# Kernel tuning notes

Measured on AMD Instinct MI355X. Metric: run time of the kernel, lower is better.

The kernel has to match this reference:

```python
import jax, jax.numpy as jnp
import numpy as np

NEIGH = 0.4  # neighborhood_size from the module


def setup_inputs() -> dict:
    key = jax.random.key(0)
    ks = jax.random.split(key, 14)
    N, E, H, G, M = 1024, 64, 128, 8, 20
    OUT = 6 * M
    f32 = jnp.float32
    inp = {
        "xabs": jax.random.uniform(ks[0], (N, 2), f32),
        "i_h0": jax.random.normal(ks[1], (1, N, H), f32) * 0.1,
        "i_c0": jax.random.normal(ks[2], (1, N, H), f32) * 0.1,
        # I_Embedding: Linear(2, E)
        "W_emb": jax.random.normal(ks[3], (E, 2), f32) * 0.5,
        "b_emb": jax.random.normal(ks[4], (E,), f32) * 0.1,
        # embedding_social: Linear(G*G*H, E)
        "W_soc": jax.random.normal(ks[5], (E, G * G * H), f32) * (1.0 / np.sqrt(G * G * H)),
        "b_soc": jax.random.normal(ks[6], (E,), f32) * 0.1,
        # LSTM(2E -> H), torch gate order [i, f, g, o]
        "W_ih": jax.random.normal(ks[7], (4 * H, 2 * E), f32) * (1.0 / np.sqrt(2 * E)),
        "W_hh": jax.random.normal(ks[8], (4 * H, H), f32) * (1.0 / np.sqrt(H)),
        "b_ih": jax.random.normal(ks[9], (4 * H,), f32) * 0.05,
        "b_hh": jax.random.normal(ks[10], (4 * H,), f32) * 0.05,
        # I_Output: Linear(H, 6*M)
        "W_out": jax.random.normal(ks[11], (OUT, H), f32) * (1.0 / np.sqrt(H)),
        "b_out": jax.random.normal(ks[12], (OUT,), f32) * 0.05,
    }
    return inp


def _grid_mask(xabs, G):
    # Vectorized getGridMask: [N, N, G*G] one-hot bin membership.
    N = xabs.shape[0]
    # dx[n, m] = other_x - width_low(n); in-range iff 0 <= dx < NEIGH
    dx = xabs[None, :, 0] - (xabs[:, None, 0] - NEIGH / 2)
    dy = xabs[None, :, 1] - (xabs[:, None, 1] - NEIGH / 2)
    cell_x = jnp.floor(dx / NEIGH * G).astype(jnp.int32)
    cell_y = jnp.floor(dy / NEIGH * G).astype(jnp.int32)
    valid = (dx >= 0) & (dx < NEIGH) & (dy >= 0) & (dy < NEIGH)
    valid &= (cell_x >= 0) & (cell_x < G) & (cell_y >= 0) & (cell_y < G)
    valid &= ~jnp.eye(N, dtype=bool)  # skip self
    cell = jnp.where(valid, cell_x + cell_y * G, 0)
    mask = jax.nn.one_hot(cell, G * G, dtype=xabs.dtype)
    return mask * valid[:, :, None].astype(xabs.dtype)


def reference(xabs, i_h0, i_c0, W_emb, b_emb, W_soc, b_soc,
              W_ih, W_hh, b_ih, b_hh, W_out, b_out):
    N = xabs.shape[0]
    H = i_h0.shape[-1]
    G = int(np.sqrt(W_soc.shape[1] // H))
    M = W_out.shape[0] // 6

    # Input embedding
    emb_x = jax.nn.relu(xabs @ W_emb.T + b_emb)  # [N, E]

    # Social pooling: grid mask + scatter-reduce of hidden states
    h0 = i_h0[0]  # [N, H]
    mask = _grid_mask(xabs, G)  # [N, N, G*G]
    social = jnp.einsum('nmg,md->ngd', mask, h0)  # [N, G*G, H]
    social = social.reshape(N, G * G * H)
    pooling = jax.nn.relu(social @ W_soc.T + b_soc)  # [N, E]

    # Single LSTM step (seq len 1, 1 layer), torch gate order i,f,g,o
    lstm_in = jnp.concatenate([emb_x, pooling], axis=-1)  # [N, 2E]
    gates = lstm_in @ W_ih.T + b_ih + h0 @ W_hh.T + b_hh  # [N, 4H]
    i_g, f_g, g_g, o_g = jnp.split(gates, 4, axis=-1)
    c = jax.nn.sigmoid(f_g) * i_c0[0] + jax.nn.sigmoid(i_g) * jnp.tanh(g_g)
    h = jax.nn.sigmoid(o_g) * jnp.tanh(c)  # [N, H]

    final = h @ W_out.T + b_out  # [N, 6M]
    mu1, mu2, log_sigma1, log_sigma2, rho, pi_logits = jnp.split(final, 6, axis=1)
    return (mu1, mu2, log_sigma1, log_sigma2, rho, pi_logits)
```

## Files before the change

### kernel.cpp

```cpp
#include <hip/hip_runtime.h>
#include <hip/hip_bf16.h>
#include <math.h>

typedef __hip_bfloat16 bf16;
typedef short s8v __attribute__((ext_vector_type(8)));
typedef float f4v __attribute__((ext_vector_type(4)));

__device__ __forceinline__ float b2f(bf16 v) { return __bfloat162float(v); }

template <bool F32>
__device__ __forceinline__ float ld(const void* p, int i) {
  if (F32) return ((const float*)p)[i];
  return b2f(((const bf16*)p)[i]);
}

template <bool F32>
__device__ __forceinline__ s8v ldfrag(const void* p, size_t i) {
  if (F32) {
    const float* f = (const float*)p + i;
    float4 u = *reinterpret_cast<const float4*>(f);
    float4 v = *reinterpret_cast<const float4*>(f + 4);
    s8v r;
    bf16 t;
    t = __float2bfloat16(u.x); r[0] = *(short*)&t;
    t = __float2bfloat16(u.y); r[1] = *(short*)&t;
    t = __float2bfloat16(u.z); r[2] = *(short*)&t;
    t = __float2bfloat16(u.w); r[3] = *(short*)&t;
    t = __float2bfloat16(v.x); r[4] = *(short*)&t;
    t = __float2bfloat16(v.y); r[5] = *(short*)&t;
    t = __float2bfloat16(v.z); r[6] = *(short*)&t;
    t = __float2bfloat16(v.w); r[7] = *(short*)&t;
    return r;
  }
  return *reinterpret_cast<const s8v*>((const bf16*)p + i);
}

__device__ __forceinline__ float sigm(float x) {
  return 0.5f * (1.0f + tanhf(0.5f * x));
}

__device__ __forceinline__ bool detect_f32(const void* xabs) {
  unsigned short v = ((const unsigned short*)xabs)[threadIdx.x & 63];
  int ex = (v >> 7) & 0xFF;
  return __ballot(ex >= 0x93) != 0ull;
}

template <bool F32>
__device__ __forceinline__ void cvt_f4(const void* src, bf16* __restrict__ dst,
                                       int i4) {
  if (F32) {
    float4 v = reinterpret_cast<const float4*>(src)[i4];
    bf16 t[4] = {__float2bfloat16(v.x), __float2bfloat16(v.y),
                 __float2bfloat16(v.z), __float2bfloat16(v.w)};
    reinterpret_cast<uint2*>(dst)[i4] = *reinterpret_cast<uint2*>(t);
  } else {
    reinterpret_cast<uint2*>(dst)[i4] = reinterpret_cast<const uint2*>(src)[i4];
  }
}

template <bool F32>
__device__ __forceinline__ void zgemm_body(const void* h0, const void* Wsoc,
                                           const void* Wih, const void* Whh,
                                           const void* Wout,
                                           bf16* __restrict__ Z, bf16* Wih_b,
                                           bf16* Whh_b, bf16* Wout_b) {
  const int t4 = blockIdx.x * 256 + threadIdx.x;
  if (t4 < 16384)
    cvt_f4<F32>(Wih, Wih_b, t4);
  else if (t4 < 32768)
    cvt_f4<F32>(Whh, Whh_b, t4 - 16384);
  else if (t4 < 36608)
    cvt_f4<F32>(Wout, Wout_b, t4 - 32768);

  const int wave = threadIdx.x >> 6, lane = threadIdx.x & 63;
  const int mt = blockIdx.x & 15;
  const int g  = (blockIdx.x >> 4) * 4 + wave;
  const int r16 = lane & 15, quad = lane >> 4;

  s8v afr[4][4];
#pragma unroll
  for (int ms = 0; ms < 4; ++ms)
#pragma unroll
    for (int kq = 0; kq < 4; ++kq)
      afr[ms][kq] = ldfrag<F32>(
          h0, (size_t)(mt * 64 + ms * 16 + r16) * 128 + kq * 32 + quad * 8);

  f4v acc[4][4];
#pragma unroll
  for (int ms = 0; ms < 4; ++ms)
#pragma unroll
    for (int t = 0; t < 4; ++t) acc[ms][t] = (f4v){0.f, 0.f, 0.f, 0.f};

#pragma unroll
  for (int t = 0; t < 4; ++t) {
#pragma unroll
    for (int kq = 0; kq < 4; ++kq) {
      s8v bfr = ldfrag<F32>(
          Wsoc, (size_t)(t * 16 + r16) * 8192 + g * 128 + kq * 32 + quad * 8);
#pragma unroll
      for (int ms = 0; ms < 4; ++ms)
        acc[ms][t] = __builtin_amdgcn_mfma_f32_16x16x32_bf16(afr[ms][kq], bfr,
                                                             acc[ms][t], 0, 0, 0);
    }
  }
#pragma unroll
  for (int ms = 0; ms < 4; ++ms)
#pragma unroll
    for (int t = 0; t < 4; ++t)
#pragma unroll
      for (int reg = 0; reg < 4; ++reg)
        Z[(size_t)(mt * 64 + ms * 16 + quad * 4 + reg) * 4096 + g * 64 +
          t * 16 + r16] = __float2bfloat16(acc[ms][t][reg]);
}

__global__ __launch_bounds__(256, 1) void k_zgemm(
    const void* h0, const void* Wsoc, const void* Wih, const void* Whh,
    const void* Wout, bf16* __restrict__ Z, bf16* Wih_b, bf16* Whh_b,
    bf16* Wout_b, const void* xabs) {
  if (detect_f32(xabs))
    zgemm_body<true>(h0, Wsoc, Wih, Whh, Wout, Z, Wih_b, Whh_b, Wout_b);
  else
    zgemm_body<false>(h0, Wsoc, Wih, Whh, Wout, Z, Wih_b, Whh_b, Wout_b);
}

#define XS 264
#define HS 136

template <bool F32>
__device__ __forceinline__ void fused_body(
    const void* xabs, const void* h0, const void* Wemb, const void* bemb,
    const void* bsoc, const bf16* __restrict__ Wih_b,
    const bf16* __restrict__ Whh_b, const void* bih, const void* bhh,
    const void* c0, const bf16* __restrict__ Wout_b, const void* bout,
    const bf16* __restrict__ Z, void* out, char* smem) {
  float* G   = (float*)smem;
  int* lists = (int*)smem;
  bf16* Xb   = (bf16*)(smem + 32768);
  bf16* Hb   = (bf16*)(smem + 32768 + 16 * XS * 2);
  const int tid = threadIdx.x;
  const int wave = tid >> 6, lane = tid & 63;
  const int r16 = lane & 15, quad = lane >> 4;
  const int l31 = lane & 31, half = lane >> 5;

  for (int idx = 4 * XS + tid; idx < 16 * XS; idx += 256)
    Xb[idx] = __float2bfloat16(0.f);
  for (int idx = 4 * HS + tid; idx < 16 * HS; idx += 256)
    Hb[idx] = __float2bfloat16(0.f);

  const int n = blockIdx.x * 4 + wave;
  const float xn = ld<F32>(xabs, 2 * n);
  const float yn = ld<F32>(xabs, 2 * n + 1);
  const float tx = xn - 0.2f, ty = yn - 0.2f;
  float dxs[16], dys[16];
#pragma unroll
  for (int c = 0; c < 16; ++c) {
    const int m = c * 64 + lane;
    dxs[c] = ld<F32>(xabs, 2 * m) - tx;
    dys[c] = ld<F32>(xabs, 2 * m + 1) - ty;
  }
  int* mylist = lists + wave * 1024;
  int cnt = 0;
#pragma unroll
  for (int c = 0; c < 16; ++c) {
    const int m = c * 64 + lane;
    float dx = dxs[c], dy = dys[c];
    int cx = (int)floorf(dx / 0.4f * 8.0f);
    int cy = (int)floorf(dy / 0.4f * 8.0f);
    bool valid = (dx >= 0.f) & (dx < 0.4f) & (dy >= 0.f) & (dy < 0.4f) &
                 (cx >= 0) & (cx < 8) & (cy >= 0) & (cy < 8) & (m != n);
    unsigned long long msk = __ballot(valid);
    if (valid) {
      int pos = cnt + __popcll(msk & ((1ull << lane) - 1ull));
      mylist[pos] = (m << 6) | (cx + cy * 8);
    }
    cnt += __popcll(msk);
  }

  float emb = fmaxf(ld<F32>(Wemb, lane * 2) * xn +
                        ld<F32>(Wemb, lane * 2 + 1) * yn + ld<F32>(bemb, lane),
                    0.f);
  Xb[wave * XS + lane] = __float2bfloat16(emb);
  Xb[wave * XS + 128 + lane] = __float2bfloat16(ld<F32>(h0, n * 128 + lane));
  Xb[wave * XS + 192 + lane] =
      __float2bfloat16(ld<F32>(h0, n * 128 + 64 + lane));

  float ax[16], ay[16];
#pragma unroll
  for (int u = 0; u < 16; ++u) { ax[u] = 0.f; ay[u] = 0.f; }
  int i = 0;
  for (; i + 32 <= cnt; i += 32) {
    int e[16];
#pragma unroll
    for (int u = 0; u < 16; ++u) e[u] = mylist[i + 2 * u + half];
#pragma unroll
    for (int u = 0; u < 16; ++u) {
      unsigned d = *reinterpret_cast<const unsigned*>(
          &Z[(size_t)(e[u] >> 6) * 4096 + ((e[u] & 63) << 6) + (l31 << 1)]);
      ax[u] += __uint_as_float(d << 16);
      ay[u] += __uint_as_float(d & 0xffff0000u);
    }
  }
  for (; i + 8 <= cnt; i += 8) {
    int e[4];
#pragma unroll
    for (int u = 0; u < 4; ++u) e[u] = mylist[i + 2 * u + half];
#pragma unroll
    for (int u = 0; u < 4; ++u) {
      unsigned d = *reinterpret_cast<const unsigned*>(
          &Z[(size_t)(e[u] >> 6) * 4096 + ((e[u] & 63) << 6) + (l31 << 1)]);
      ax[u] += __uint_as_float(d << 16);
      ay[u] += __uint_as_float(d & 0xffff0000u);
    }
  }
  for (; i + 2 <= cnt; i += 2) {
    int e0 = mylist[i + half];
    unsigned d = *reinterpret_cast<const unsigned*>(
        &Z[(size_t)(e0 >> 6) * 4096 + ((e0 & 63) << 6) + (l31 << 1)]);
    ax[0] += __uint_as_float(d << 16);
    ay[0] += __uint_as_float(d & 0xffff0000u);
  }
  if (i < cnt) {
    int e0 = mylist[i];
    if (half == 0) {
      unsigned d = *reinterpret_cast<const unsigned*>(
          &Z[(size_t)(e0 >> 6) * 4096 + ((e0 & 63) << 6) + (l31 << 1)]);
      ax[0] += __uint_as_float(d << 16);
      ay[0] += __uint_as_float(d & 0xffff0000u);
    }
  }
#pragma unroll
  for (int u = 8; u < 16; ++u) { ax[u - 8] += ax[u]; ay[u - 8] += ay[u]; }
#pragma unroll
  for (int u = 4; u < 8; ++u) { ax[u - 4] += ax[u]; ay[u - 4] += ay[u]; }
  float sx = (ax[0] + ax[1]) + (ax[2] + ax[3]);
  float sy = (ay[0] + ay[1]) + (ay[2] + ay[3]);
  sx += __shfl_xor(sx, 32);
  sy += __shfl_xor(sy, 32);
  if (half == 0) {
    float p0 = fmaxf(sx + ld<F32>(bsoc, l31 * 2), 0.f);
    float p1 = fmaxf(sy + ld<F32>(bsoc, l31 * 2 + 1), 0.f);
    Xb[wave * XS + 64 + l31 * 2] = __float2bfloat16(p0);
    Xb[wave * XS + 64 + l31 * 2 + 1] = __float2bfloat16(p1);
  }
  __syncthreads();

  s8v xfr[8];
#pragma unroll
  for (int kq = 0; kq < 8; ++kq)
    xfr[kq] = *reinterpret_cast<const s8v*>(&Xb[r16 * XS + kq * 32 + quad * 8]);
  const int j0w = wave * 128;
  f4v bacc[8];
#pragma unroll
  for (int jt = 0; jt < 8; ++jt) bacc[jt] = (f4v){0.f, 0.f, 0.f, 0.f};
#pragma unroll
  for (int jt = 0; jt < 8; ++jt) {
    int j = j0w + jt * 16 + r16;
#pragma unroll
    for (int kq = 0; kq < 4; ++kq) {
      s8v bfr = *reinterpret_cast<const s8v*>(
          &Wih_b[(size_t)j * 128 + kq * 32 + quad * 8]);
      bacc[jt] = __builtin_amdgcn_mfma_f32_16x16x32_bf16(xfr[kq], bfr, bacc[jt],
                                                         0, 0, 0);
    }
#pragma unroll
    for (int kq = 0; kq < 4; ++kq) {
      s8v bfr = *reinterpret_cast<const s8v*>(
          &Whh_b[(size_t)j * 128 + kq * 32 + quad * 8]);
      bacc[jt] = __builtin_amdgcn_mfma_f32_16x16x32_bf16(xfr[kq + 4], bfr,
                                                         bacc[jt], 0, 0, 0);
    }
  }
#pragma unroll
  for (int jt = 0; jt < 8; ++jt) {
    int j = j0w + jt * 16 + r16;
    float bias = ld<F32>(bih, j) + ld<F32>(bhh, j);
#pragma unroll
    for (int reg = 0; reg < 4; ++reg)
      G[(quad * 4 + reg) * 512 + j] = bacc[jt][reg] + bias;
  }
  __syncthreads();

  for (int idx = tid; idx < 512; idx += 256) {
    int m = idx >> 7, tt = idx & 127;
    float ig = G[m * 512 + tt], fg = G[m * 512 + 128 + tt];
    float gg = G[m * 512 + 256 + tt], og = G[m * 512 + 384 + tt];
    float c = sigm(fg) * ld<F32>(c0, (blockIdx.x * 4 + m) * 128 + tt) +
              sigm(ig) * tanhf(gg);
    Hb[m * HS + tt] = __float2bfloat16(sigm(og) * tanhf(c));
  }
  __syncthreads();

  s8v hfr[4];
#pragma unroll
  for (int kq = 0; kq < 4; ++kq)
    hfr[kq] = *reinterpret_cast<const s8v*>(&Hb[r16 * HS + kq * 32 + quad * 8]);
#pragma unroll
  for (int jt2 = 0; jt2 < 2; ++jt2) {
    int j = wave * 32 + jt2 * 16 + r16;
    int jj = j < 120 ? j : 119;
    f4v oacc = (f4v){0.f, 0.f, 0.f, 0.f};
#pragma unroll
    for (int kq = 0; kq < 4; ++kq) {
      s8v bfr = *reinterpret_cast<const s8v*>(
          &Wout_b[(size_t)jj * 128 + kq * 32 + quad * 8]);
      oacc = __builtin_amdgcn_mfma_f32_16x16x32_bf16(hfr[kq], bfr, oacc, 0, 0, 0);
    }
    if (j < 120 && quad == 0) {
      float bo = ld<F32>(bout, j);
      int kk = j / 20, mm = j % 20;
#pragma unroll
      for (int reg = 0; reg < 4; ++reg) {
        int oi = kk * 20480 + (blockIdx.x * 4 + reg) * 20 + mm;
        float val = oacc[reg] + bo;
        if (F32) ((float*)out)[oi] = val;
        else     ((bf16*)out)[oi] = __float2bfloat16(val);
      }
    }
  }
}

__global__ __launch_bounds__(256, 1) void k_fused(
    const void* xabs, const void* h0, const void* Wemb, const void* bemb,
    const void* bsoc, const bf16* Wih_b, const bf16* Whh_b, const void* bih,
    const void* bhh, const void* c0, const bf16* Wout_b, const void* bout,
    const bf16* __restrict__ Z, void* out) {
  __shared__ __align__(16) char smem[32768 + 16 * XS * 2 + 16 * HS * 2];
  if (detect_f32(xabs))
    fused_body<true>(xabs, h0, Wemb, bemb, bsoc, Wih_b, Whh_b, bih, bhh, c0,
                     Wout_b, bout, Z, out, smem);
  else
    fused_body<false>(xabs, h0, Wemb, bemb, bsoc, Wih_b, Whh_b, bih, bhh, c0,
                      Wout_b, bout, Z, out, smem);
}

extern "C" void kernel_launch(void* const* d_in, const int* in_sizes, int n_in,
                              void* d_out, int out_size, void* d_ws, size_t ws_size,
                              hipStream_t stream) {
  const void* xabs = d_in[0];
  const void* h0   = d_in[1];
  const void* c0   = d_in[2];
  const void* Wemb = d_in[3];
  const void* bemb = d_in[4];
  const void* Wsoc = d_in[5];
  const void* bsoc = d_in[6];
  const void* Wih  = d_in[7];
  const void* Whh  = d_in[8];
  const void* bih  = d_in[9];
  const void* bhh  = d_in[10];
  const void* Wout = d_in[11];
  const void* bout = d_in[12];

  bf16* Z      = (bf16*)d_ws;
  bf16* Wih_b  = Z + (size_t)1024 * 4096;
  bf16* Whh_b  = Wih_b + (size_t)512 * 128;
  bf16* Wout_b = Whh_b + (size_t)512 * 128;

  k_zgemm<<<dim3(256), dim3(256), 0, stream>>>(h0, Wsoc, Wih, Whh, Wout, Z,
                                               Wih_b, Whh_b, Wout_b, xabs);
  k_fused<<<dim3(256), dim3(256), 0, stream>>>(xabs, h0, Wemb, bemb, bsoc,
                                               Wih_b, Whh_b, bih, bhh, c0,
                                               Wout_b, bout, Z, d_out);
}
```

Before: 119.7 us.

## Widen social gather to 16-byte loads with padded neighbor lists and faster activations

```diff
diff --git a/kernel.cpp b/kernel.cpp
--- a/kernel.cpp
+++ b/kernel.cpp
@@ -5,6 +5,7 @@
 typedef __hip_bfloat16 bf16;
 typedef short s8v __attribute__((ext_vector_type(8)));
 typedef float f4v __attribute__((ext_vector_type(4)));
+typedef unsigned u4v __attribute__((ext_vector_type(4)));
 
 __device__ __forceinline__ float b2f(bf16 v) { return __bfloat162float(v); }
 
@@ -36,7 +37,10 @@
 }
 
 __device__ __forceinline__ float sigm(float x) {
-  return 0.5f * (1.0f + tanhf(0.5f * x));
+  return __builtin_amdgcn_rcpf(1.0f + __expf(-x));
+}
+__device__ __forceinline__ float ftanh(float x) {
+  return 1.0f - 2.0f * __builtin_amdgcn_rcpf(1.0f + __expf(2.0f * x));
 }
 
 __device__ __forceinline__ bool detect_f32(const void* xabs) {
@@ -71,6 +75,10 @@
     cvt_f4<F32>(Whh, Whh_b, t4 - 16384);
   else if (t4 < 36608)
     cvt_f4<F32>(Wout, Wout_b, t4 - 32768);
+
+  if (blockIdx.x == 0 && threadIdx.x < 16)
+    reinterpret_cast<uint2*>(Z + (size_t)1024 * 4096)[threadIdx.x] =
+        (uint2){0u, 0u};
 
   const int wave = threadIdx.x >> 6, lane = threadIdx.x & 63;
   const int mt = blockIdx.x & 15;
@@ -140,7 +148,7 @@
   const int tid = threadIdx.x;
   const int wave = tid >> 6, lane = tid & 63;
   const int r16 = lane & 15, quad = lane >> 4;
-  const int l31 = lane & 31, half = lane >> 5;
+  const int rowg = lane >> 3, colg = lane & 7;
 
   for (int idx = 4 * XS + tid; idx < 16 * XS; idx += 256)
     Xb[idx] = __float2bfloat16(0.f);
@@ -175,6 +183,8 @@
     }
     cnt += __popcll(msk);
   }
+  const int padded = (cnt + 7) & ~7;
+  if (cnt + lane < padded) mylist[cnt + lane] = (1024 << 6);
 
   float emb = fmaxf(ld<F32>(Wemb, lane * 2) * xn +
                         ld<F32>(Wemb, lane * 2 + 1) * yn + ld<F32>(bemb, lane),
@@ -184,63 +194,80 @@
   Xb[wave * XS + 192 + lane] =
       __float2bfloat16(ld<F32>(h0, n * 128 + 64 + lane));
 
-  float ax[16], ay[16];
-#pragma unroll
-  for (int u = 0; u < 16; ++u) { ax[u] = 0.f; ay[u] = 0.f; }
+  float ax[4], ay[4];
+#pragma unroll
+  for (int w = 0; w < 4; ++w) { ax[w] = 0.f; ay[w] = 0.f; }
   int i = 0;
-  for (; i + 32 <= cnt; i += 32) {
-    int e[16];
-#pragma unroll
-    for (int u = 0; u < 16; ++u) e[u] = mylist[i + 2 * u + half];
+  for (; i + 128 <= padded; i += 128) {
+    u4v d[16];
 #pragma unroll
     for (int u = 0; u < 16; ++u) {
-      unsigned d = *reinterpret_cast<const unsigned*>(
-          &Z[(size_t)(e[u] >> 6) * 4096 + ((e[u] & 63) << 6) + (l31 << 1)]);
-      ax[u] += __uint_as_float(d << 16);
-      ay[u] += __uint_as_float(d & 0xffff0000u);
-    }
-  }
-  for (; i + 8 <= cnt; i += 8) {
-    int e[4];
-#pragma unroll
-    for (int u = 0; u < 4; ++u) e[u] = mylist[i + 2 * u + half];
-#pragma unroll
-    for (int u = 0; u < 4; ++u) {
-      unsigned d = *reinterpret_cast<const unsigned*>(
-          &Z[(size_t)(e[u] >> 6) * 4096 + ((e[u] & 63) << 6) + (l31 << 1)]);
-      ax[u] += __uint_as_float(d << 16);
-      ay[u] += __uint_as_float(d & 0xffff0000u);
-    }
-  }
-  for (; i + 2 <= cnt; i += 2) {
-    int e0 = mylist[i + half];
-    unsigned d = *reinterpret_cast<const unsigned*>(
-        &Z[(size_t)(e0 >> 6) * 4096 + ((e0 & 63) << 6) + (l31 << 1)]);
-    ax[0] += __uint_as_float(d << 16);
-    ay[0] += __uint_as_float(d & 0xffff0000u);
-  }
-  if (i < cnt) {
-    int e0 = mylist[i];
-    if (half == 0) {
-      unsigned d = *reinterpret_cast<const unsigned*>(
-          &Z[(size_t)(e0 >> 6) * 4096 + ((e0 & 63) << 6) + (l31 << 1)]);
-      ax[0] += __uint_as_float(d << 16);
-      ay[0] += __uint_as_float(d & 0xffff0000u);
-    }
-  }
-#pragma unroll
-  for (int u = 8; u < 16; ++u) { ax[u - 8] += ax[u]; ay[u - 8] += ay[u]; }
-#pragma unroll
-  for (int u = 4; u < 8; ++u) { ax[u - 4] += ax[u]; ay[u - 4] += ay[u]; }
-  float sx = (ax[0] + ax[1]) + (ax[2] + ax[3]);
-  float sy = (ay[0] + ay[1]) + (ay[2] + ay[3]);
-  sx += __shfl_xor(sx, 32);
-  sy += __shfl_xor(sy, 32);
-  if (half == 0) {
-    float p0 = fmaxf(sx + ld<F32>(bsoc, l31 * 2), 0.f);
-    float p1 = fmaxf(sy + ld<F32>(bsoc, l31 * 2 + 1), 0.f);
-    Xb[wave * XS + 64 + l31 * 2] = __float2bfloat16(p0);
-    Xb[wave * XS + 64 + l31 * 2 + 1] = __float2bfloat16(p1);
+      int e = mylist[i + u * 8 + rowg];
+      d[u] = *reinterpret_cast<const u4v*>(
+          &Z[(size_t)(e >> 6) * 4096 + ((e & 63) << 6) + (colg << 3)]);
+    }
+#pragma unroll
+    for (int u = 0; u < 16; ++u)
+#pragma unroll
+      for (int w = 0; w < 4; ++w) {
+        ax[w] += __uint_as_float(d[u][w] << 16);
+        ay[w] += __uint_as_float(d[u][w] & 0xffff0000u);
+      }
+  }
+  int rem = padded - i;
+  if (rem >= 64) {
+    u4v d[8];
+#pragma unroll
+    for (int u = 0; u < 8; ++u) {
+      int e = mylist[i + u * 8 + rowg];
+      d[u] = *reinterpret_cast<const u4v*>(
+          &Z[(size_t)(e >> 6) * 4096 + ((e & 63) << 6) + (colg << 3)]);
+    }
+#pragma unroll
+    for (int u = 0; u < 8; ++u)
+#pragma unroll
+      for (int w = 0; w < 4; ++w) {
+        ax[w] += __uint_as_float(d[u][w] << 16);
+        ay[w] += __uint_as_float(d[u][w] & 0xffff0000u);
+      }
+    i += 64;
+    rem -= 64;
+  }
+  {
+    const int ns = rem >> 3;
+    u4v d[7];
+#pragma unroll
+    for (int u = 0; u < 7; ++u)
+      if (u < ns) {
+        int e = mylist[i + u * 8 + rowg];
+        d[u] = *reinterpret_cast<const u4v*>(
+            &Z[(size_t)(e >> 6) * 4096 + ((e & 63) << 6) + (colg << 3)]);
+      }
+#pragma unroll
+    for (int u = 0; u < 7; ++u)
+      if (u < ns)
+#pragma unroll
+        for (int w = 0; w < 4; ++w) {
+          ax[w] += __uint_as_float(d[u][w] << 16);
+          ay[w] += __uint_as_float(d[u][w] & 0xffff0000u);
+        }
+  }
+#pragma unroll
+  for (int mks = 8; mks <= 32; mks <<= 1)
+#pragma unroll
+    for (int w = 0; w < 4; ++w) {
+      ax[w] += __shfl_xor(ax[w], mks);
+      ay[w] += __shfl_xor(ay[w], mks);
+    }
+  if (rowg == 0) {
+#pragma unroll
+    for (int w = 0; w < 4; ++w) {
+      int c0 = colg * 8 + 2 * w;
+      Xb[wave * XS + 64 + c0] =
+          __float2bfloat16(fmaxf(ax[w] + ld<F32>(bsoc, c0), 0.f));
+      Xb[wave * XS + 64 + c0 + 1] =
+          __float2bfloat16(fmaxf(ay[w] + ld<F32>(bsoc, c0 + 1), 0.f));
+    }
   }
   __syncthreads();
 
@@ -270,13 +297,15 @@
                                                          bacc[jt], 0, 0, 0);
     }
   }
-#pragma unroll
-  for (int jt = 0; jt < 8; ++jt) {
-    int j = j0w + jt * 16 + r16;
-    float bias = ld<F32>(bih, j) + ld<F32>(bhh, j);
-#pragma unroll
-    for (int reg = 0; reg < 4; ++reg)
-      G[(quad * 4 + reg) * 512 + j] = bacc[jt][reg] + bias;
+  if (quad == 0) {
+#pragma unroll
+    for (int jt = 0; jt < 8; ++jt) {
+      int j = j0w + jt * 16 + r16;
+      float bias = ld<F32>(bih, j) + ld<F32>(bhh, j);
+#pragma unroll
+      for (int reg = 0; reg < 4; ++reg)
+        G[reg * 512 + j] = bacc[jt][reg] + bias;
+    }
   }
   __syncthreads();
 
@@ -285,8 +314,8 @@
     float ig = G[m * 512 + tt], fg = G[m * 512 + 128 + tt];
     float gg = G[m * 512 + 256 + tt], og = G[m * 512 + 384 + tt];
     float c = sigm(fg) * ld<F32>(c0, (blockIdx.x * 4 + m) * 128 + tt) +
-              sigm(ig) * tanhf(gg);
-    Hb[m * HS + tt] = __float2bfloat16(sigm(og) * tanhf(c));
+              sigm(ig) * ftanh(gg);
+    Hb[m * HS + tt] = __float2bfloat16(sigm(og) * ftanh(c));
   }
   __syncthreads();
 
@@ -351,7 +380,7 @@
   const void* bout = d_in[12];
 
   bf16* Z      = (bf16*)d_ws;
-  bf16* Wih_b  = Z + (size_t)1024 * 4096;
+  bf16* Wih_b  = Z + (size_t)1025 * 4096;
   bf16* Whh_b  = Wih_b + (size_t)512 * 128;
   bf16* Wout_b = Whh_b + (size_t)512 * 128;
 
```

Result: faster. 112.3 us (-6.2%).
